# Kernel tuning notes

Measured on AMD Instinct MI355X. Metric: run time of the kernel, lower is better.

The kernel has to match this reference:

```python
import jax, jax.numpy as jnp
import numpy as np

N_NODES = 100000
IN_C, HID_C, OUT_C = 128, 64, 5
NEG_SLOPE = 0.01  # F.leaky_relu default


def gcn_conv(x, W, b, src_sl, dst_sl, norm, n_nodes):
    """PyG GCNConv: h = D^{-1/2}(A+I)D^{-1/2} (x W) + b.
    src_sl/dst_sl already include self-loops; norm is the per-edge coefficient."""
    h = x @ W                              # [N, out]
    msg = h[src_sl] * norm[:, None]        # [E+N, out] gather + scale
    agg = jax.ops.segment_sum(msg, dst_sl, num_segments=n_nodes)
    return agg + b


def setup_inputs() -> dict:
    key = jax.random.key(0)
    ks = jax.random.split(key, 8)
    n, e = N_NODES, 1600000
    x = jax.random.normal(ks[0], (n, IN_C), dtype=jnp.float32)
    edge_index = jax.random.randint(ks[1], (2, e), 0, n, dtype=jnp.int64)
    idx = jax.random.randint(ks[2], (20000,), 0, n, dtype=jnp.int64)
    # Glorot-ish init for GCNConv weights, kaiming-ish for MLP
    W0 = jax.random.normal(ks[3], (IN_C, HID_C), dtype=jnp.float32) * (1.0 / np.sqrt(IN_C))
    b0 = jnp.zeros((HID_C,), dtype=jnp.float32)
    W1 = jax.random.normal(ks[4], (HID_C, HID_C), dtype=jnp.float32) * (1.0 / np.sqrt(HID_C))
    b1 = jnp.zeros((HID_C,), dtype=jnp.float32)
    Wm = jax.random.normal(ks[5], (HID_C, OUT_C), dtype=jnp.float32) * (1.0 / np.sqrt(HID_C))
    bm = jnp.zeros((OUT_C,), dtype=jnp.float32)
    return {"x": x, "edge_index": edge_index, "idx": idx,
            "W0": W0, "b0": b0, "W1": W1, "b1": b1, "Wm": Wm, "bm": bm}


def reference(x, edge_index, idx, W0, b0, W1, b1, Wm, bm):
    n = x.shape[0]
    src, dst = edge_index[0], edge_index[1]
    loops = jnp.arange(n, dtype=edge_index.dtype)
    src_sl = jnp.concatenate([src, loops])
    dst_sl = jnp.concatenate([dst, loops])
    # symmetric normalization with self-loops (gcn_norm)
    deg = jax.ops.segment_sum(jnp.ones_like(dst_sl, dtype=x.dtype), dst_sl, num_segments=n)
    dinv = jnp.where(deg > 0, jax.lax.rsqrt(deg), 0.0)
    norm = dinv[src_sl] * dinv[dst_sl]     # [E+N]

    h = jax.nn.leaky_relu(gcn_conv(x, W0, b0, src_sl, dst_sl, norm, n), NEG_SLOPE)
    h = jax.nn.leaky_relu(gcn_conv(h, W1, b1, src_sl, dst_sl, norm, n), NEG_SLOPE)

    h_sel = h[idx]                          # index_select on node dim
    out = jax.nn.sigmoid(h_sel @ Wm + bm)
    return (h_sel, out)
```

## Files before the change

kernel.cpp:

```cpp
#include <hip/hip_runtime.h>
#include <hip/hip_fp16.h>
#include <math.h>


#define NPART 64
#define MAXB 2048

typedef _Float16 h8 __attribute__((ext_vector_type(8)));
typedef float f4v __attribute__((ext_vector_type(4)));

__device__ __forceinline__ float lrelu(float x) { return x > 0.0f ? x : 0.01f * x; }


__global__ __launch_bounds__(1024) void k_part_hist(const int* __restrict__ dst, int E,
                                                    int B, int* __restrict__ phist) {
    __shared__ int scnt[MAXB];
    int t = threadIdx.x, p = blockIdx.x;
    for (int i = t; i < B; i += 1024) scnt[i] = 0;
    __syncthreads();
    int ep = (((E + NPART - 1) / NPART) + 3) & ~3;
    int beg = p * ep, endi = min(E, beg + ep);
    int cnt4 = (endi - beg) >> 2;
    for (int i = t; i < cnt4; i += 1024) {
        int4 d = *(const int4*)(dst + beg + i * 4);
        atomicAdd(&scnt[d.x >> 6], 1);
        atomicAdd(&scnt[d.y >> 6], 1);
        atomicAdd(&scnt[d.z >> 6], 1);
        atomicAdd(&scnt[d.w >> 6], 1);
    }
    int rem = (endi - beg) & 3;
    if (t < rem) atomicAdd(&scnt[dst[beg + cnt4 * 4 + t] >> 6], 1);
    __syncthreads();
    for (int i = t; i < B; i += 1024) phist[i * NPART + p] = scnt[i];
}

__global__ __launch_bounds__(1024) void k_part_scatter(const int* __restrict__ src,
                                                       const int* __restrict__ dst, int E,
                                                       int B, const int* __restrict__ pbase,
                                                       int* __restrict__ esA) {
    __shared__ int sbase[MAXB];
    int t = threadIdx.x, p = blockIdx.x;
    for (int i = t; i < B; i += 1024) sbase[i] = pbase[i * NPART + p];
    __syncthreads();
    int ep = (((E + NPART - 1) / NPART) + 3) & ~3;
    int beg = p * ep, endi = min(E, beg + ep);
    int cnt4 = (endi - beg) >> 2;
    for (int i = t; i < cnt4; i += 1024) {
        int e = beg + i * 4;
        int4 d = *(const int4*)(dst + e);
        int4 s = *(const int4*)(src + e);
        int p0 = atomicAdd(&sbase[d.x >> 6], 1);
        int p1 = atomicAdd(&sbase[d.y >> 6], 1);
        int p2 = atomicAdd(&sbase[d.z >> 6], 1);
        int p3 = atomicAdd(&sbase[d.w >> 6], 1);
        esA[p0] = ((d.x & 63) << 24) | s.x;
        esA[p1] = ((d.y & 63) << 24) | s.y;
        esA[p2] = ((d.z & 63) << 24) | s.z;
        esA[p3] = ((d.w & 63) << 24) | s.w;
    }
    int rem = (endi - beg) & 3;
    if (t < rem) {
        int e = beg + cnt4 * 4 + t;
        int d = dst[e];
        int pos = atomicAdd(&sbase[d >> 6], 1);
        esA[pos] = ((d & 63) << 24) | src[e];
    }
}


__global__ void k_blocksum(const int* __restrict__ cnt, int N, int* __restrict__ bsum) {
    __shared__ int sm[256];
    int b = blockIdx.x, t = threadIdx.x;
    int base = b * 1024 + t * 4;
    int s = 0;
#pragma unroll
    for (int i = 0; i < 4; ++i) { int j = base + i; if (j < N) s += cnt[j]; }
    sm[t] = s; __syncthreads();
    for (int off = 128; off > 0; off >>= 1) {
        if (t < off) sm[t] += sm[t + off];
        __syncthreads();
    }
    if (t == 0) bsum[b] = sm[0];
}

__global__ void k_scan_bsum(int* __restrict__ bsum, int nb, int* __restrict__ offN) {
    __shared__ int sm[1024];
    int t = threadIdx.x;
    int v = (t < nb) ? bsum[t] : 0;
    sm[t] = v; __syncthreads();
    for (int d = 1; d < 1024; d <<= 1) {
        int add = (t >= d) ? sm[t - d] : 0;
        __syncthreads();
        sm[t] += add;
        __syncthreads();
    }
    if (t < nb) bsum[t] = sm[t] - v;
    if (t == nb - 1) *offN = sm[t];
}

__global__ void k_scan_block(const int* __restrict__ cnt, const int* __restrict__ bsum,
                             int* __restrict__ off, int N) {
    __shared__ int sm[256];
    int b = blockIdx.x, t = threadIdx.x;
    int base = b * 1024 + t * 4;
    int v[4];
#pragma unroll
    for (int i = 0; i < 4; ++i) { int j = base + i; v[i] = (j < N) ? cnt[j] : 0; }
    int tsum = v[0] + v[1] + v[2] + v[3];
    sm[t] = tsum; __syncthreads();
    for (int d = 1; d < 256; d <<= 1) {
        int val = (t >= d) ? sm[t - d] : 0;
        __syncthreads();
        sm[t] += val;
        __syncthreads();
    }
    int run = sm[t] - tsum + bsum[b];
#pragma unroll
    for (int i = 0; i < 4; ++i) {
        int j = base + i;
        if (j < N) off[j] = run;
        run += v[i];
    }
}


__global__ __launch_bounds__(256) void k_bsort(const int* __restrict__ pbase, int BP,
                                               const int* __restrict__ esA,
                                               int* __restrict__ esB,
                                               int* __restrict__ off,
                                               float* __restrict__ dinv,
                                               int N, int E) {
    __shared__ int hcnt[64];
    __shared__ int hoff[64];
    int t = threadIdx.x, b = blockIdx.x;
    int start = pbase[b * NPART];
    int endi  = pbase[min((b + 1) * NPART, BP)];
    int cnt = endi - start;

    if (t < 64) hcnt[t] = 0;
    __syncthreads();
    for (int i = t * 4; i < cnt; i += 1024) {
#pragma unroll
        for (int c = 0; c < 4; ++c)
            if (i + c < cnt) atomicAdd(&hcnt[(esA[start + i + c] >> 24) & 63], 1);
    }
    __syncthreads();

    if (t < 64) {
        int c = hcnt[t];
        int v = c;
#pragma unroll
        for (int d = 1; d < 64; d <<= 1) {
            int u = __shfl_up(v, d);
            if (t >= d) v += u;
        }
        int pos = start + (v - c);
        hoff[t] = pos;
        int g = b * 64 + t;
        if (g < N) {
            off[g] = pos;
            dinv[g] = rsqrtf((float)c + 1.0f);
        }
        if (g == N - 1) off[N] = E;
    }
    __syncthreads();
    if (t < 64) hcnt[t] = hoff[t];
    __syncthreads();

    for (int i = t * 4; i < cnt; i += 1024) {
#pragma unroll
        for (int c = 0; c < 4; ++c)
            if (i + c < cnt) {
                int v = esA[start + i + c];
                int pos = atomicAdd(&hcnt[(v >> 24) & 63], 1);
                esB[pos] = v & 0xFFFFFF;
            }
    }
}


template <int K, typename AT>
__global__ __launch_bounds__(256) void k_gemm(const AT* __restrict__ A,
                                              const float* __restrict__ W,
                                              const float* __restrict__ dinv,
                                              __half* __restrict__ hout, int N) {
    constexpr int ASTR = K + 8;
    __shared__ _Float16 a16[64 * ASTR];
    __shared__ _Float16 wt16[64 * ASTR];
    int t = threadIdx.x, lane = t & 63, wv = t >> 6;
    int rowBase = blockIdx.x * 64;

#pragma unroll
    for (int i = 0; i < K / 16; ++i) {
        int g = i * 256 + t;
        int r = g / (K / 4), kq = g % (K / 4);
        int gr = rowBase + r; if (gr >= N) gr = N - 1;
        _Float16* p = a16 + r * ASTR + kq * 4;
        if constexpr (sizeof(AT) == 4) {
            float4 v = *(const float4*)((const float*)A + (size_t)gr * K + kq * 4);
            *(__half2*)(p)     = __floats2half2_rn(v.x, v.y);
            *(__half2*)(p + 2) = __floats2half2_rn(v.z, v.w);
        } else {
            *(uint2*)p = *(const uint2*)((const __half*)A + (size_t)gr * K + kq * 4);
        }
    }
#pragma unroll
    for (int i = 0; i < K / 16; ++i) {
        int g = i * 256 + t;
        int k = g >> 4, nq = g & 15;
        float4 v = *(const float4*)(W + (size_t)k * 64 + nq * 4);
        wt16[(nq * 4 + 0) * ASTR + k] = (_Float16)v.x;
        wt16[(nq * 4 + 1) * ASTR + k] = (_Float16)v.y;
        wt16[(nq * 4 + 2) * ASTR + k] = (_Float16)v.z;
        wt16[(nq * 4 + 3) * ASTR + k] = (_Float16)v.w;
    }
    __syncthreads();

    int m = lane & 15, q = lane >> 4;
    f4v acc[4] = {{0,0,0,0},{0,0,0,0},{0,0,0,0},{0,0,0,0}};
    const _Float16* arow = a16 + (wv * 16 + m) * ASTR + q * 8;
#pragma unroll
    for (int kt = 0; kt < K / 32; ++kt) {
        h8 af = *(const h8*)(arow + kt * 32);
#pragma unroll
        for (int nt = 0; nt < 4; ++nt) {
            h8 bf = *(const h8*)(wt16 + (nt * 16 + m) * ASTR + kt * 32 + q * 8);
            acc[nt] = __builtin_amdgcn_mfma_f32_16x16x32_f16(af, bf, acc[nt], 0, 0, 0);
        }
    }

    int r0 = rowBase + wv * 16 + q * 4;
#pragma unroll
    for (int reg = 0; reg < 4; ++reg) {
        int row = r0 + reg;
        if (row >= N) continue;
        float dv = dinv[row];
#pragma unroll
        for (int nt = 0; nt < 4; ++nt)
            hout[(size_t)row * 64 + nt * 16 + m] = (__half)(acc[nt][reg] * dv);
    }
}


__global__ __launch_bounds__(256) void k_agg1(const int* __restrict__ off,
                                              const int* __restrict__ esB,
                                              const float* __restrict__ dinv,
                                              const __half* __restrict__ hs,
                                              const float* __restrict__ b0,
                                              __half* __restrict__ aout, int N) {
    int lane = threadIdx.x & 63;
    int node = (blockIdx.x * blockDim.x + threadIdx.x) >> 6;
    if (node >= N) return;
    int qt = lane >> 4, l16 = lane & 15;
    int beg = off[node], end = off[node + 1];

    float ax = 0, ay = 0, az = 0, aw = 0;
    auto ld = [&](int s) { return *(const uint2*)(hs + (size_t)s * 64 + l16 * 4); };
    auto acc4 = [&](uint2 u) {
        float2 f0 = __half22float2(*(__half2*)&u.x);
        float2 f1 = __half22float2(*(__half2*)&u.y);
        ax += f0.x; ay += f0.y; az += f1.x; aw += f1.y;
    };
    if (qt == 0) acc4(ld(node));
    int j = beg + qt;
    for (; j + 12 < end; j += 16) {
        int s0 = esB[j], s1 = esB[j + 4], s2 = esB[j + 8], s3 = esB[j + 12];
        uint2 u0 = ld(s0), u1 = ld(s1), u2 = ld(s2), u3 = ld(s3);
        acc4(u0); acc4(u1); acc4(u2); acc4(u3);
    }
    for (; j < end; j += 4) acc4(ld(esB[j]));

#pragma unroll
    for (int d = 16; d <= 32; d <<= 1) {
        ax += __shfl_xor(ax, d); ay += __shfl_xor(ay, d);
        az += __shfl_xor(az, d); aw += __shfl_xor(aw, d);
    }
    if (qt == 0) {
        float dv = dinv[node];
        float4 b = *(const float4*)(b0 + l16 * 4);
        float ox = lrelu(ax * dv + b.x), oy = lrelu(ay * dv + b.y);
        float oz = lrelu(az * dv + b.z), ow = lrelu(aw * dv + b.w);
        uint2 u;
        *(__half2*)&u.x = __floats2half2_rn(ox, oy);
        *(__half2*)&u.y = __floats2half2_rn(oz, ow);
        *(uint2*)(aout + (size_t)node * 64 + l16 * 4) = u;
    }
}


__global__ __launch_bounds__(256) void k_aggout(const int* __restrict__ idx,
                                                const int* __restrict__ off,
                                                const int* __restrict__ esB,
                                                const float* __restrict__ dinv,
                                                const __half* __restrict__ hs,
                                                const float* __restrict__ b1,
                                                const float* __restrict__ Wm,
                                                const float* __restrict__ bm,
                                                float* __restrict__ out, int NSEL) {
    int lane = threadIdx.x & 63;
    int wv = (blockIdx.x * blockDim.x + threadIdx.x) >> 6;
    if (wv >= NSEL) return;
    int node = idx[wv];
    int qt = lane >> 4, l16 = lane & 15;
    int beg = off[node], end = off[node + 1];

    float ax = 0, ay = 0, az = 0, aw = 0;
    auto ld = [&](int s) { return *(const uint2*)(hs + (size_t)s * 64 + l16 * 4); };
    auto acc4 = [&](uint2 u) {
        float2 f0 = __half22float2(*(__half2*)&u.x);
        float2 f1 = __half22float2(*(__half2*)&u.y);
        ax += f0.x; ay += f0.y; az += f1.x; aw += f1.y;
    };
    if (qt == 0) acc4(ld(node));
    int j = beg + qt;
    for (; j + 12 < end; j += 16) {
        int s0 = esB[j], s1 = esB[j + 4], s2 = esB[j + 8], s3 = esB[j + 12];
        uint2 u0 = ld(s0), u1 = ld(s1), u2 = ld(s2), u3 = ld(s3);
        acc4(u0); acc4(u1); acc4(u2); acc4(u3);
    }
    for (; j < end; j += 4) acc4(ld(esB[j]));

#pragma unroll
    for (int d = 16; d <= 32; d <<= 1) {
        ax += __shfl_xor(ax, d); ay += __shfl_xor(ay, d);
        az += __shfl_xor(az, d); aw += __shfl_xor(aw, d);
    }

    float dv = dinv[node];
    float4 b = *(const float4*)(b1 + l16 * 4);
    float4 hsel;
    hsel.x = lrelu(ax * dv + b.x); hsel.y = lrelu(ay * dv + b.y);
    hsel.z = lrelu(az * dv + b.z); hsel.w = lrelu(aw * dv + b.w);
    if (qt == 0) *(float4*)(out + (size_t)wv * 64 + l16 * 4) = hsel;

    const float* wr = Wm + (size_t)(4 * l16) * 5;
#pragma unroll
    for (int o = 0; o < 5; ++o) {
        float p = hsel.x * wr[o] + hsel.y * wr[5 + o] +
                  hsel.z * wr[10 + o] + hsel.w * wr[15 + o];
        p += __shfl_xor(p, 1); p += __shfl_xor(p, 2);
        p += __shfl_xor(p, 4); p += __shfl_xor(p, 8);
        if (lane == 0)
            out[(size_t)NSEL * 64 + (size_t)wv * 5 + o] =
                1.0f / (1.0f + expf(-(p + bm[o])));
    }
}

extern "C" void kernel_launch(void* const* d_in, const int* in_sizes, int n_in,
                              void* d_out, int out_size, void* d_ws, size_t ws_size,
                              hipStream_t stream) {
    const float* x   = (const float*)d_in[0];
    const int*   ei  = (const int*)d_in[1];
    const int*   idx = (const int*)d_in[2];
    const float* W0  = (const float*)d_in[3];
    const float* b0  = (const float*)d_in[4];
    const float* W1  = (const float*)d_in[5];
    const float* b1  = (const float*)d_in[6];
    const float* Wm  = (const float*)d_in[7];
    const float* bm  = (const float*)d_in[8];

    int N    = in_sizes[0] / 128;
    int E    = in_sizes[1] / 2;
    int NSEL = in_sizes[2];
    const int* src = ei;
    const int* dst = ei + E;

    int B  = (N + 63) / 64;
    int BP = B * NPART;

    char* w = (char*)d_ws;
    size_t Na  = ((size_t)N + 1023) & ~(size_t)1023;
    size_t Ea  = ((size_t)E + 1023) & ~(size_t)1023;
    size_t BPa = ((size_t)BP + 1023) & ~(size_t)1023;
    float*  dinv  = (float*)w;                w += Na * 4;
    int*    phist = (int*)w;                  w += BPa * 4;
    int*    pbase = (int*)w;                  w += (BPa + 1024) * 4;
    int*    bsum  = (int*)w;                  w += 1024 * 4;
    int*    off   = (int*)w;                  w += (Na + 1024) * 4;
    int*    esA   = (int*)w;                  w += Ea * 4;
    int*    esB   = (int*)w;                  w += Ea * 4;
    __half* hs16  = (__half*)w;               w += (size_t)N * 64 * 2;
    __half* a16g  = (__half*)w;

    int nbp = (BP + 1023) / 1024;

    k_part_hist<<<NPART, 1024, 0, stream>>>(dst, E, B, phist);
    k_blocksum<<<nbp, 256, 0, stream>>>(phist, BP, bsum);
    k_scan_bsum<<<1, 1024, 0, stream>>>(bsum, nbp, pbase + BP);
    k_scan_block<<<nbp, 256, 0, stream>>>(phist, bsum, pbase, BP);
    k_part_scatter<<<NPART, 1024, 0, stream>>>(src, dst, E, B, pbase, esA);
    k_bsort<<<B, 256, 0, stream>>>(pbase, BP, esA, esB, off, dinv, N, E);

    int gemm_blocks = (N + 63) / 64;
    int agg_blocks  = (N + 3) / 4;

    k_gemm<128, float><<<gemm_blocks, 256, 0, stream>>>(x, W0, dinv, hs16, N);
    k_agg1<<<agg_blocks, 256, 0, stream>>>(off, esB, dinv, hs16, b0, a16g, N);
    k_gemm<64, __half><<<gemm_blocks, 256, 0, stream>>>(a16g, W1, dinv, hs16, N);
    k_aggout<<<(NSEL + 3) / 4, 256, 0, stream>>>(idx, off, esB, dinv, hs16, b1, Wm, bm,
                                                 (float*)d_out, NSEL);
}
```

Baseline: 259.2 us.

## Widen aggregation gathers to 16-byte loads and raise partition count

The aggregation kernels now have each group of 8 lanes read a full 128-byte fp16 row with uint4 loads, instead of 16 lanes each issuing 8-byte loads, so 8 edges are processed per wave step instead of 4. This cuts the number of gather instructions and the unroll depth per lane, at the cost of more shuffle reductions (8 values across 3 steps). Separately, the edge partitioning now uses 256 partitions instead of 64 to spread the histogram and scatter work over more blocks. The added length clamp guards partitions that receive no edges.

```diff
diff --git a/kernel.cpp b/kernel.cpp
--- a/kernel.cpp
+++ b/kernel.cpp
@@ -3,7 +3,7 @@
 #include <math.h>
 
 
-#define NPART 64
+#define NPART 256
 #define MAXB 2048
 
 typedef _Float16 h8 __attribute__((ext_vector_type(8)));
@@ -20,7 +20,8 @@
     __syncthreads();
     int ep = (((E + NPART - 1) / NPART) + 3) & ~3;
     int beg = p * ep, endi = min(E, beg + ep);
-    int cnt4 = (endi - beg) >> 2;
+    int len = endi - beg; if (len < 0) len = 0;
+    int cnt4 = len >> 2;
     for (int i = t; i < cnt4; i += 1024) {
         int4 d = *(const int4*)(dst + beg + i * 4);
         atomicAdd(&scnt[d.x >> 6], 1);
@@ -28,7 +29,7 @@
         atomicAdd(&scnt[d.z >> 6], 1);
         atomicAdd(&scnt[d.w >> 6], 1);
     }
-    int rem = (endi - beg) & 3;
+    int rem = len & 3;
     if (t < rem) atomicAdd(&scnt[dst[beg + cnt4 * 4 + t] >> 6], 1);
     __syncthreads();
     for (int i = t; i < B; i += 1024) phist[i * NPART + p] = scnt[i];
@@ -44,7 +45,8 @@
     __syncthreads();
     int ep = (((E + NPART - 1) / NPART) + 3) & ~3;
     int beg = p * ep, endi = min(E, beg + ep);
-    int cnt4 = (endi - beg) >> 2;
+    int len = endi - beg; if (len < 0) len = 0;
+    int cnt4 = len >> 2;
     for (int i = t; i < cnt4; i += 1024) {
         int e = beg + i * 4;
         int4 d = *(const int4*)(dst + e);
@@ -58,7 +60,7 @@
         esA[p2] = ((d.z & 63) << 24) | s.z;
         esA[p3] = ((d.w & 63) << 24) | s.w;
     }
-    int rem = (endi - beg) & 3;
+    int rem = len & 3;
     if (t < rem) {
         int e = beg + cnt4 * 4 + t;
         int d = dst[e];
@@ -251,39 +253,43 @@
     int lane = threadIdx.x & 63;
     int node = (blockIdx.x * blockDim.x + threadIdx.x) >> 6;
     if (node >= N) return;
-    int qt = lane >> 4, l16 = lane & 15;
+    int oct = lane >> 3, l8 = lane & 7;
     int beg = off[node], end = off[node + 1];
 
-    float ax = 0, ay = 0, az = 0, aw = 0;
-    auto ld = [&](int s) { return *(const uint2*)(hs + (size_t)s * 64 + l16 * 4); };
-    auto acc4 = [&](uint2 u) {
+    float a[8] = {0, 0, 0, 0, 0, 0, 0, 0};
+    auto ld = [&](int s) { return *(const uint4*)(hs + (size_t)s * 64 + l8 * 8); };
+    auto acc8 = [&](uint4 u) {
         float2 f0 = __half22float2(*(__half2*)&u.x);
         float2 f1 = __half22float2(*(__half2*)&u.y);
-        ax += f0.x; ay += f0.y; az += f1.x; aw += f1.y;
+        float2 f2 = __half22float2(*(__half2*)&u.z);
+        float2 f3 = __half22float2(*(__half2*)&u.w);
+        a[0] += f0.x; a[1] += f0.y; a[2] += f1.x; a[3] += f1.y;
+        a[4] += f2.x; a[5] += f2.y; a[6] += f3.x; a[7] += f3.y;
     };
-    if (qt == 0) acc4(ld(node));
-    int j = beg + qt;
-    for (; j + 12 < end; j += 16) {
-        int s0 = esB[j], s1 = esB[j + 4], s2 = esB[j + 8], s3 = esB[j + 12];
-        uint2 u0 = ld(s0), u1 = ld(s1), u2 = ld(s2), u3 = ld(s3);
-        acc4(u0); acc4(u1); acc4(u2); acc4(u3);
-    }
-    for (; j < end; j += 4) acc4(ld(esB[j]));
-
-#pragma unroll
-    for (int d = 16; d <= 32; d <<= 1) {
-        ax += __shfl_xor(ax, d); ay += __shfl_xor(ay, d);
-        az += __shfl_xor(az, d); aw += __shfl_xor(aw, d);
-    }
-    if (qt == 0) {
+    if (oct == 0) acc8(ld(node));
+    int j = beg + oct;
+    for (; j + 8 < end; j += 16) {
+        int s0 = esB[j], s1 = esB[j + 8];
+        uint4 u0 = ld(s0), u1 = ld(s1);
+        acc8(u0); acc8(u1);
+    }
+    if (j < end) acc8(ld(esB[j]));
+
+#pragma unroll
+    for (int d = 8; d <= 32; d <<= 1) {
+#pragma unroll
+        for (int i = 0; i < 8; ++i) a[i] += __shfl_xor(a[i], d);
+    }
+    if (oct == 0) {
         float dv = dinv[node];
-        float4 b = *(const float4*)(b0 + l16 * 4);
-        float ox = lrelu(ax * dv + b.x), oy = lrelu(ay * dv + b.y);
-        float oz = lrelu(az * dv + b.z), ow = lrelu(aw * dv + b.w);
-        uint2 u;
-        *(__half2*)&u.x = __floats2half2_rn(ox, oy);
-        *(__half2*)&u.y = __floats2half2_rn(oz, ow);
-        *(uint2*)(aout + (size_t)node * 64 + l16 * 4) = u;
+        float4 bl = *(const float4*)(b0 + l8 * 8);
+        float4 bh = *(const float4*)(b0 + l8 * 8 + 4);
+        uint4 u;
+        *(__half2*)&u.x = __floats2half2_rn(lrelu(a[0] * dv + bl.x), lrelu(a[1] * dv + bl.y));
+        *(__half2*)&u.y = __floats2half2_rn(lrelu(a[2] * dv + bl.z), lrelu(a[3] * dv + bl.w));
+        *(__half2*)&u.z = __floats2half2_rn(lrelu(a[4] * dv + bh.x), lrelu(a[5] * dv + bh.y));
+        *(__half2*)&u.w = __floats2half2_rn(lrelu(a[6] * dv + bh.z), lrelu(a[7] * dv + bh.w));
+        *(uint4*)(aout + (size_t)node * 64 + l8 * 8) = u;
     }
 }
 
@@ -301,45 +307,56 @@
     int wv = (blockIdx.x * blockDim.x + threadIdx.x) >> 6;
     if (wv >= NSEL) return;
     int node = idx[wv];
-    int qt = lane >> 4, l16 = lane & 15;
+    int oct = lane >> 3, l8 = lane & 7;
     int beg = off[node], end = off[node + 1];
 
-    float ax = 0, ay = 0, az = 0, aw = 0;
-    auto ld = [&](int s) { return *(const uint2*)(hs + (size_t)s * 64 + l16 * 4); };
-    auto acc4 = [&](uint2 u) {
+    float a[8] = {0, 0, 0, 0, 0, 0, 0, 0};
+    auto ld = [&](int s) { return *(const uint4*)(hs + (size_t)s * 64 + l8 * 8); };
+    auto acc8 = [&](uint4 u) {
         float2 f0 = __half22float2(*(__half2*)&u.x);
         float2 f1 = __half22float2(*(__half2*)&u.y);
-        ax += f0.x; ay += f0.y; az += f1.x; aw += f1.y;
+        float2 f2 = __half22float2(*(__half2*)&u.z);
+        float2 f3 = __half22float2(*(__half2*)&u.w);
+        a[0] += f0.x; a[1] += f0.y; a[2] += f1.x; a[3] += f1.y;
+        a[4] += f2.x; a[5] += f2.y; a[6] += f3.x; a[7] += f3.y;
     };
-    if (qt == 0) acc4(ld(node));
-    int j = beg + qt;
-    for (; j + 12 < end; j += 16) {
-        int s0 = esB[j], s1 = esB[j + 4], s2 = esB[j + 8], s3 = esB[j + 12];
-        uint2 u0 = ld(s0), u1 = ld(s1), u2 = ld(s2), u3 = ld(s3);
-        acc4(u0); acc4(u1); acc4(u2); acc4(u3);
-    }
-    for (; j < end; j += 4) acc4(ld(esB[j]));
-
-#pragma unroll
-    for (int d = 16; d <= 32; d <<= 1) {
-        ax += __shfl_xor(ax, d); ay += __shfl_xor(ay, d);
-        az += __shfl_xor(az, d); aw += __shfl_xor(aw, d);
+    if (oct == 0) acc8(ld(node));
+    int j = beg + oct;
+    for (; j + 8 < end; j += 16) {
+        int s0 = esB[j], s1 = esB[j + 8];
+        uint4 u0 = ld(s0), u1 = ld(s1);
+        acc8(u0); acc8(u1);
+    }
+    if (j < end) acc8(ld(esB[j]));
+
+#pragma unroll
+    for (int d = 8; d <= 32; d <<= 1) {
+#pragma unroll
+        for (int i = 0; i < 8; ++i) a[i] += __shfl_xor(a[i], d);
     }
 
     float dv = dinv[node];
-    float4 b = *(const float4*)(b1 + l16 * 4);
-    float4 hsel;
-    hsel.x = lrelu(ax * dv + b.x); hsel.y = lrelu(ay * dv + b.y);
-    hsel.z = lrelu(az * dv + b.z); hsel.w = lrelu(aw * dv + b.w);
-    if (qt == 0) *(float4*)(out + (size_t)wv * 64 + l16 * 4) = hsel;
-
-    const float* wr = Wm + (size_t)(4 * l16) * 5;
+    float4 bl = *(const float4*)(b1 + l8 * 8);
+    float4 bh = *(const float4*)(b1 + l8 * 8 + 4);
+    float hsel[8];
+    hsel[0] = lrelu(a[0] * dv + bl.x); hsel[1] = lrelu(a[1] * dv + bl.y);
+    hsel[2] = lrelu(a[2] * dv + bl.z); hsel[3] = lrelu(a[3] * dv + bl.w);
+    hsel[4] = lrelu(a[4] * dv + bh.x); hsel[5] = lrelu(a[5] * dv + bh.y);
+    hsel[6] = lrelu(a[6] * dv + bh.z); hsel[7] = lrelu(a[7] * dv + bh.w);
+    if (oct == 0) {
+        float4 o0 = {hsel[0], hsel[1], hsel[2], hsel[3]};
+        float4 o1 = {hsel[4], hsel[5], hsel[6], hsel[7]};
+        *(float4*)(out + (size_t)wv * 64 + l8 * 8) = o0;
+        *(float4*)(out + (size_t)wv * 64 + l8 * 8 + 4) = o1;
+    }
+
+    const float* wr = Wm + (size_t)(8 * l8) * 5;
 #pragma unroll
     for (int o = 0; o < 5; ++o) {
-        float p = hsel.x * wr[o] + hsel.y * wr[5 + o] +
-                  hsel.z * wr[10 + o] + hsel.w * wr[15 + o];
-        p += __shfl_xor(p, 1); p += __shfl_xor(p, 2);
-        p += __shfl_xor(p, 4); p += __shfl_xor(p, 8);
+        float p = 0.0f;
+#pragma unroll
+        for (int i = 0; i < 8; ++i) p = fmaf(hsel[i], wr[i * 5 + o], p);
+        p += __shfl_xor(p, 1); p += __shfl_xor(p, 2); p += __shfl_xor(p, 4);
         if (lane == 0)
             out[(size_t)NSEL * 64 + (size_t)wv * 5 + o] =
                 1.0f / (1.0f + expf(-(p + bm[o])));
```

Result: no change. 263.9 us (+1.8%).
